# Kernel optimization log

Hardware: AMD Instinct MI355X
Metric: run time of the kernel (lower is better)

The kernel has to match this reference:

```python
import jax, jax.numpy as jnp
import numpy as np

B, C, H, W = 512, 256, 9, 9
HEADS, K = 4, 9
D_K = C // HEADS
EPS = 1e-5


def setup_inputs() -> dict:
    key = jax.random.key(0)
    ks = jax.random.split(key, 8)
    s = 1.0 / np.sqrt(C)
    return {
        "x": jax.random.normal(ks[0], (B, C, H, W), jnp.float32),
        "wq": jax.random.normal(ks[1], (C, C), jnp.float32) * s,
        "bq": jax.random.normal(ks[2], (C,), jnp.float32) * s,
        "wk": jax.random.normal(ks[3], (C, C), jnp.float32) * s,
        "bk": jax.random.normal(ks[4], (C,), jnp.float32) * s,
        "wv": jax.random.normal(ks[5], (C, C), jnp.float32) * s,
        "bv": jax.random.normal(ks[6], (C,), jnp.float32) * s,
        "a": jax.random.normal(ks[7], (HEADS, D_K), jnp.float32),
        "gamma": jnp.ones((C,), jnp.float32),
        "beta": jnp.zeros((C,), jnp.float32),
    }


def reference(x, wq, bq, wk, bk, wv, bv, a, gamma, beta):
    N = H * W  # 81 tokens
    tokens = x.reshape(B, C, N).transpose(0, 2, 1)  # [B, N, C]

    # pairwise euclidean distances (cdist)
    sq = jnp.sum(tokens * tokens, axis=-1)  # [B, N]
    d2 = sq[:, :, None] + sq[:, None, :] - 2.0 * jnp.einsum("bnc,bmc->bnm", tokens, tokens)
    dist = jnp.sqrt(jnp.maximum(d2, 0.0))  # [B, N, N]

    # k nearest neighbors (smallest distance)
    _, idx = jax.lax.top_k(-dist, K)  # idx: [B, N, K]

    # gather neighbor features: [B, N, K, C]
    nbr = jax.vmap(lambda t, i: t[i])(tokens, idx)

    q = tokens @ wq.T + bq                      # [B, N, C]
    kf = nbr @ wk.T + bk                        # [B, N, K, C]
    comb = jax.nn.leaky_relu(q[:, :, None, :] + kf, 0.2)
    comb = comb.reshape(B, N, K, HEADS, D_K)
    scores = jnp.einsum("bnkhd,hd->bnkh", comb, a)
    attn = jax.nn.softmax(scores, axis=2)       # over K neighbors
    v = (nbr @ wv.T + bv).reshape(B, N, K, HEADS, D_K)
    out = jnp.einsum("bnkh,bnkhd->bnhd", attn, v).reshape(B, N, C)
    out = out.transpose(0, 2, 1).reshape(B, C, H, W)

    # BatchNorm2d (training-mode batch statistics, biased variance)
    mean = jnp.mean(out, axis=(0, 2, 3))
    var = jnp.var(out, axis=(0, 2, 3))
    bn = (out - mean[None, :, None, None]) * jax.lax.rsqrt(var + EPS)[None, :, None, None]
    bn = bn * gamma[None, :, None, None] + beta[None, :, None, None]
    return jax.nn.relu(bn + x)
```

## Files before the change

### kernel.cpp

```cpp
#include <hip/hip_runtime.h>
#include <hip/hip_bf16.h>

#define B_   512
#define C_   256
#define N_   81
#define M_   (B_ * N_)
#define KNN  9

typedef __attribute__((ext_vector_type(8))) short short8;
typedef __attribute__((ext_vector_type(4))) float f32x4;
typedef __attribute__((ext_vector_type(4))) ushort u16x4;

#define GLD16(g, l) __builtin_amdgcn_global_load_lds(                      \
    (const __attribute__((address_space(1))) void*)(g),                    \
    (__attribute__((address_space(3))) void*)(l), 16, 0, 0)

__device__ __forceinline__ float bf2f(ushort u) {
  union { uint i; float f; } c; c.i = (uint)u << 16; return c.f;
}
__device__ __forceinline__ ushort f2bf(float f) {
  __hip_bfloat16 h = __float2bfloat16(f); return *(ushort*)&h;
}

__global__ __launch_bounds__(256) void split_kernel(
    const float* __restrict__ x, ushort* __restrict__ tokb,
    char* __restrict__ lobuf,
    const float* __restrict__ wq, const float* __restrict__ bq,
    const float* __restrict__ wk, const float* __restrict__ bk,
    const float* __restrict__ wv, const float* __restrict__ bv,
    ushort* __restrict__ wcat, float* __restrict__ bcat) {
  __shared__ __align__(16) float raw[32 * 81];
  const int bid = blockIdx.x;
  const int tid = threadIdx.x;
  if (bid >= 4096) {
    const int j = bid - 4096, c = tid;
    const int sel = j >> 8, jr = j & 255;
    const float* W  = sel == 0 ? wq : (sel == 1 ? wk : wv);
    const float* Bb = sel == 0 ? bq : (sel == 1 ? bk : bv);
    wcat[(size_t)j * 256 + c] = f2bf(W[jr * 256 + c]);
    if (c == 0) bcat[j] = Bb[jr];
    return;
  }
  const int b = bid >> 3, ch = bid & 7;
  const float* src = x + (size_t)b * (C_ * N_) + ch * 32 * N_;
#pragma unroll
  for (int it = 0; it < 3; ++it) {
    int e4 = tid + it * 256;
    if (e4 < 648) *(f32x4*)&raw[e4 * 4] = *(const f32x4*)&src[e4 * 4];
  }
  char* dst = lobuf + (size_t)bid * 6144;
  __syncthreads();
#pragma unroll
  for (int it = 0; it < 6; ++it) {
    int p = tid + it * 256;
    if (p < 1296) {
      int n = p >> 4, q = p & 15;
      float v0 = raw[(2 * q) * N_ + n];
      float v1 = raw[(2 * q + 1) * N_ + n];
      __hip_bfloat16 h0 = __float2bfloat16(v0);
      __hip_bfloat16 h1 = __float2bfloat16(v1);
      float r0 = v0 - __bfloat162float(h0);
      float r1 = v1 - __bfloat162float(h1);
      __hip_bfloat16 g0 = __float2bfloat16(r0);
      __hip_bfloat16 g1 = __float2bfloat16(r1);
      uint hp = (uint)(*(ushort*)&h0) | ((uint)(*(ushort*)&h1) << 16);
      uint lp = (uint)(*(ushort*)&g0) | ((uint)(*(ushort*)&g1) << 16);
      int off = (((q >> 2) << 4) ^ (((n >> 1) & 3) << 4)) + ((q & 3) << 2);
      *(uint*)(dst + n * 64 + off) = lp;
      *(uint*)&tokb[((size_t)(b * N_ + n)) * 256 + ch * 32 + 2 * q] = hp;
    }
  }
}

__global__ __launch_bounds__(256) void knn_gemm_kernel(
    const ushort* __restrict__ tokb, const char* __restrict__ lobuf,
    int* __restrict__ knn_idx,
    const ushort* __restrict__ wcat, const float* __restrict__ bcat,
    ushort* __restrict__ qkvb) {
  __shared__ __align__(16) char smem[32768];
  const int bid0 = blockIdx.x;
  const int tid = threadIdx.x;
  const int w = tid >> 6, lane = tid & 63;
  const int l15 = lane & 15;

  if (bid0 < B_) {
    float* sqv = (float*)(smem + 31488);
    const int b = bid0;
    const int wr = w >> 1, wc = w & 1;
    const int g16 = lane >> 4;

    const char* tb = (const char*)(tokb + (size_t)b * N_ * 256);
    const char* lb = lobuf + (size_t)b * 8 * 6144;

#pragma unroll
    for (int it = 0; it < 3; ++it) {
      int idx = it * 256 + tid;
      if (idx < 384) {
        int n = idx >> 2, gp = idx & 3;
        int g = gp ^ ((n >> 1) & 3);
        GLD16(tb + (size_t)n * 512 + (g << 4), smem + idx * 16);
      } else {
        GLD16(lb + (idx - 384) * 16, smem + idx * 16);
      }
    }

    f32x4 acc[3][3];
#pragma unroll
    for (int i = 0; i < 3; ++i)
#pragma unroll
      for (int j = 0; j < 3; ++j) acc[i][j] = {0.f, 0.f, 0.f, 0.f};

#pragma unroll
    for (int ch = 0; ch < 8; ++ch) {
      char* cur = smem + (ch & 1) * 12288;
      char* nxt = smem + ((ch + 1) & 1) * 12288;
      if (ch < 7) {
#pragma unroll
        for (int it = 0; it < 3; ++it) {
          int idx = it * 256 + tid;
          if (idx < 384) {
            int n = idx >> 2, gp = idx & 3;
            int g = gp ^ ((n >> 1) & 3);
            GLD16(tb + (size_t)n * 512 + (ch + 1) * 64 + (g << 4),
                  nxt + idx * 16);
          } else {
            GLD16(lb + (size_t)(ch + 1) * 6144 + (idx - 384) * 16,
                  nxt + idx * 16);
          }
        }
        asm volatile("s_waitcnt vmcnt(3)" ::: "memory");
      } else {
        asm volatile("s_waitcnt vmcnt(0)" ::: "memory");
      }
      __builtin_amdgcn_s_barrier();
      __builtin_amdgcn_sched_barrier(0);
      short8 ah[3], al[3], bh[3], bl[3];
#pragma unroll
      for (int i = 0; i < 3; ++i) {
        int ra = wr * 48 + i * 16 + l15;
        int oa = ra * 64 + ((g16 << 4) ^ (((ra >> 1) & 3) << 4));
        ah[i] = *(const short8*)(cur + oa);
        al[i] = *(const short8*)(cur + 6144 + oa);
        int rb = wc * 48 + i * 16 + l15;
        int ob = rb * 64 + ((g16 << 4) ^ (((rb >> 1) & 3) << 4));
        bh[i] = *(const short8*)(cur + ob);
        bl[i] = *(const short8*)(cur + 6144 + ob);
      }
#pragma unroll
      for (int i = 0; i < 3; ++i)
#pragma unroll
        for (int j = 0; j < 3; ++j) {
          acc[i][j] = __builtin_amdgcn_mfma_f32_16x16x32_bf16(
              ah[i], bh[j], acc[i][j], 0, 0, 0);
          acc[i][j] = __builtin_amdgcn_mfma_f32_16x16x32_bf16(
              ah[i], bl[j], acc[i][j], 0, 0, 0);
          acc[i][j] = __builtin_amdgcn_mfma_f32_16x16x32_bf16(
              al[i], bh[j], acc[i][j], 0, 0, 0);
          acc[i][j] = __builtin_amdgcn_mfma_f32_16x16x32_bf16(
              al[i], bl[j], acc[i][j], 0, 0, 0);
        }
      __builtin_amdgcn_sched_barrier(0);
      __builtin_amdgcn_s_barrier();
    }
    float* G = (float*)smem;
#pragma unroll
    for (int i = 0; i < 3; ++i) {
      const int row0 = wr * 48 + i * 16 + ((lane >> 4) << 2);
#pragma unroll
      for (int j = 0; j < 3; ++j) {
        const int col = wc * 48 + j * 16 + l15;
#pragma unroll
        for (int reg = 0; reg < 4; ++reg) {
          const int row = row0 + reg;
          if (row < N_) G[row * 97 + col] = acc[i][j][reg];
        }
      }
    }
    __syncthreads();
    if (tid < N_) sqv[tid] = G[tid * 97 + tid];
    __syncthreads();
    if (tid < N_) {
      const int n = tid;
      const float sn = sqv[n];
      const float* grow = &G[n * 97];
      float bd[KNN]; int bi[KNN];
#pragma unroll
      for (int k = 0; k < KNN; ++k) { bd[k] = 3.4e38f; bi[k] = 0; }
      for (int m = 0; m < N_; ++m) {
        float d2 = sn + sqv[m] - 2.f * grow[m];
        float wv = bd[0]; int wi = 0;
#pragma unroll
        for (int k = 1; k < KNN; ++k) {
          bool g_ = bd[k] > wv;
          wv = g_ ? bd[k] : wv;
          wi = g_ ? k : wi;
        }
        bool repl = d2 < wv;
#pragma unroll
        for (int k = 0; k < KNN; ++k) {
          bool here = repl & (wi == k);
          bd[k] = here ? d2 : bd[k];
          bi[k] = here ? m : bi[k];
        }
      }
#pragma unroll
      for (int k = 0; k < KNN; ++k)
        knn_idx[((size_t)b * N_ + n) * KNN + k] = bi[k];
    }
    return;
  }

  ushort* At = (ushort*)smem;
  ushort* Bt = (ushort*)(smem + 16384);
  const int bid = bid0 - B_;
  const int xcd = bid & 7, li = bid >> 3;
  const int mt = xcd * 41 + li / 6;
  if (mt >= 324) return;
  const int m0 = mt * 128;
  const int j0 = (li % 6) * 128;
  const int wr = w >> 1, wc = w & 1;

  const char* pA[4]; const char* pB[4]; int oL[4];
#pragma unroll
  for (int it = 0; it < 4; ++it) {
    int o = (it * 256 + tid) * 16;
    int r = o >> 7, cp = o & 127;
    int cl = cp ^ ((r & 7) << 4);
    oL[it] = o;
    pA[it] = (const char*)tokb + ((size_t)(m0 + r) * 256) * 2 + cl;
    pB[it] = (const char*)wcat + ((size_t)(j0 + r) * 256) * 2 + cl;
  }

  f32x4 acc[4][4];
#pragma unroll
  for (int i = 0; i < 4; ++i)
#pragma unroll
    for (int j = 0; j < 4; ++j) acc[i][j] = {0.f, 0.f, 0.f, 0.f};

  const int sw = (lane & 7) << 4;
  const int kgrp = (lane >> 4) << 4;

  for (int k0 = 0; k0 < 256; k0 += 64) {
    __syncthreads();
#pragma unroll
    for (int it = 0; it < 4; ++it) {
      GLD16(pA[it] + k0 * 2, (char*)At + oL[it]);
      GLD16(pB[it] + k0 * 2, (char*)Bt + oL[it]);
    }
    __syncthreads();
#pragma unroll
    for (int kk = 0; kk < 2; ++kk) {
      const int cb = (kk * 64 + kgrp) ^ sw;
      short8 am[4], bn[4];
#pragma unroll
      for (int i = 0; i < 4; ++i) {
        const int ra = wr * 64 + i * 16 + l15;
        am[i] = *(const short8*)((const char*)At + ra * 128 + cb);
        const int rb = wc * 64 + i * 16 + l15;
        bn[i] = *(const short8*)((const char*)Bt + rb * 128 + cb);
      }
#pragma unroll
      for (int i = 0; i < 4; ++i)
#pragma unroll
        for (int j = 0; j < 4; ++j)
          acc[i][j] = __builtin_amdgcn_mfma_f32_16x16x32_bf16(
              am[i], bn[j], acc[i][j], 0, 0, 0);
    }
  }

#pragma unroll
  for (int j = 0; j < 4; ++j) {
    const int colj = j0 + wc * 64 + j * 16 + l15;
    const float bs = bcat[colj];
#pragma unroll
    for (int i = 0; i < 4; ++i) {
      const int rowm = m0 + wr * 64 + i * 16 + ((lane >> 4) << 2);
#pragma unroll
      for (int reg = 0; reg < 4; ++reg)
        qkvb[(size_t)(rowm + reg) * 768 + colj] = f2bf(acc[i][j][reg] + bs);
    }
  }
}

__global__ __launch_bounds__(256) void attn_kernel(
    const ushort* __restrict__ qkvc, const int* __restrict__ knn_idx,
    const float* __restrict__ a, ushort* __restrict__ qkvb) {
  const int nwg = M_ / 4;
  const int bid = blockIdx.x;
  const int swz = (bid & 7) * (nwg / 8) + (bid >> 3);
  const int w = threadIdx.x >> 6, lane = threadIdx.x & 63;
  const int m = swz * 4 + w;
  const int b = m / N_;
  const int bbase = b * N_;

  int nbk_l = 0;
  if (lane < KNN) nbk_l = knn_idx[(size_t)m * KNN + lane];

  const u16x4 qu = *(const u16x4*)&qkvc[(size_t)m * 768 + lane * 4];
  const f32x4 a4 = *(const f32x4*)&a[lane * 4];
  float q4[4];
#pragma unroll
  for (int u = 0; u < 4; ++u) q4[u] = bf2f(qu[u]);

  u16x4 ku[KNN], vu[KNN];
#pragma unroll
  for (int k = 0; k < KNN; ++k) {
    const int nbk = __builtin_amdgcn_readlane(nbk_l, k);
    const ushort* row = qkvc + (size_t)(bbase + nbk) * 768;
    ku[k] = *(const u16x4*)&row[256 + lane * 4];
    vu[k] = *(const u16x4*)&row[512 + lane * 4];
  }

  float sc[KNN];
#pragma unroll
  for (int k = 0; k < KNN; ++k) {
    float p = 0.f;
#pragma unroll
    for (int u = 0; u < 4; ++u) {
      float t = q4[u] + bf2f(ku[k][u]);
      t = fmaxf(t, 0.2f * t);
      p = __builtin_fmaf(t, a4[u], p);
    }
    p += __shfl_xor(p, 1, 16);
    p += __shfl_xor(p, 2, 16);
    p += __shfl_xor(p, 4, 16);
    p += __shfl_xor(p, 8, 16);
    sc[k] = p;
  }
  float mx = sc[0];
#pragma unroll
  for (int k = 1; k < KNN; ++k) mx = fmaxf(mx, sc[k]);
  float s = 0.f;
#pragma unroll
  for (int k = 0; k < KNN; ++k) {
    sc[k] = __builtin_amdgcn_exp2f((sc[k] - mx) * 1.44269504f);
    s += sc[k];
  }
  const float inv = __builtin_amdgcn_rcpf(s);
  f32x4 acc = {0.f, 0.f, 0.f, 0.f};
#pragma unroll
  for (int k = 0; k < KNN; ++k) {
    const float wk_ = sc[k] * inv;
#pragma unroll
    for (int u = 0; u < 4; ++u)
      acc[u] = __builtin_fmaf(wk_, bf2f(vu[k][u]), acc[u]);
  }
  u16x4 o;
#pragma unroll
  for (int u = 0; u < 4; ++u) o[u] = f2bf(acc[u]);
  *(u16x4*)&qkvb[(size_t)m * 768 + lane * 4] = o;
}

__global__ __launch_bounds__(256) void bn_partial_kernel(
    const ushort* __restrict__ qkvb, float* __restrict__ ps,
    float* __restrict__ ps2) {
  const int g = blockIdx.x, c = threadIdx.x;
  float s = 0.f, s2 = 0.f;
  for (int r = 0; r < M_ / 256; ++r) {
    float v = bf2f(qkvb[((size_t)g * (M_ / 256) + r) * 768 + c]);
    s += v; s2 += v * v;
  }
  ps[g * 256 + c] = s;
  ps2[g * 256 + c] = s2;
}

__global__ __launch_bounds__(256) void bn_finalize_kernel(
    const float* __restrict__ ps, const float* __restrict__ ps2,
    const float* __restrict__ gamma, const float* __restrict__ beta,
    float* __restrict__ scale, float* __restrict__ shift) {
  __shared__ float red[2][256];
  const int c = blockIdx.x, t = threadIdx.x;
  red[0][t] = ps[t * 256 + c];
  red[1][t] = ps2[t * 256 + c];
  __syncthreads();
#pragma unroll
  for (int off = 128; off > 0; off >>= 1) {
    if (t < off) {
      red[0][t] += red[0][t + off];
      red[1][t] += red[1][t + off];
    }
    __syncthreads();
  }
  if (t == 0) {
    const float mean = red[0][0] * (1.f / (float)M_);
    const float var = red[1][0] * (1.f / (float)M_) - mean * mean;
    const float rstd = rsqrtf(var + 1e-5f);
    scale[c] = gamma[c] * rstd;
    shift[c] = beta[c] - mean * gamma[c] * rstd;
  }
}

__global__ __launch_bounds__(256) void bn_apply_kernel(
    const ushort* __restrict__ qkvb, const float* __restrict__ x,
    const float* __restrict__ scale, const float* __restrict__ shift,
    float* __restrict__ y) {
  __shared__ float t[N_ * 65];
  const int b = blockIdx.x, tid = threadIdx.x;
  for (int c0 = 0; c0 < 256; c0 += 64) {
    __syncthreads();
    for (int e = tid; e < N_ * 64; e += 256) {
      int n = e >> 6, c = e & 63;
      t[n * 65 + c] = bf2f(qkvb[((size_t)b * N_ + n) * 768 + c0 + c]);
    }
    __syncthreads();
    for (int f = tid; f < 64 * N_; f += 256) {
      int c = f / N_, n = f - c * N_;
      float o = t[n * 65 + c];
      size_t gi = (size_t)b * (C_ * N_) + (size_t)(c0 + c) * N_ + n;
      float bn = o * scale[c0 + c] + shift[c0 + c];
      float v = bn + x[gi];
      y[gi] = v > 0.f ? v : 0.f;
    }
  }
}

extern "C" void kernel_launch(void* const* d_in, const int* in_sizes, int n_in,
                              void* d_out, int out_size, void* d_ws,
                              size_t ws_size, hipStream_t stream) {
  const float* x     = (const float*)d_in[0];
  const float* wq    = (const float*)d_in[1];
  const float* bq    = (const float*)d_in[2];
  const float* wk    = (const float*)d_in[3];
  const float* bk    = (const float*)d_in[4];
  const float* wv    = (const float*)d_in[5];
  const float* bv    = (const float*)d_in[6];
  const float* a     = (const float*)d_in[7];
  const float* gamma = (const float*)d_in[8];
  const float* beta  = (const float*)d_in[9];
  float* out = (float*)d_out;

  ushort* qkvb = (ushort*)d_ws;
  char*   lobuf = (char*)qkvb;
  ushort* tokb = qkvb + (size_t)M_ * 768;
  ushort* wcat = tokb + (size_t)M_ * 256;
  float*  bcat = (float*)(wcat + 768 * 256);
  int*    kidx = (int*)(bcat + 768);
  float*  ps   = (float*)(kidx + (size_t)M_ * KNN);
  float*  ps2  = ps + 256 * 256;
  float*  scale = ps2 + 256 * 256;
  float*  shift = scale + 256;
  char*   lobuf2 = (char*)(shift + 256);

  split_kernel<<<4096 + 768, 256, 0, stream>>>(
      x, tokb, lobuf2, wq, bq, wk, bk, wv, bv, wcat, bcat);
  knn_gemm_kernel<<<B_ + 1968, 256, 0, stream>>>(
      tokb, lobuf2, kidx, wcat, bcat, qkvb);
  attn_kernel<<<M_ / 4, 256, 0, stream>>>(qkvb, kidx, a, qkvb);
  bn_partial_kernel<<<256, 256, 0, stream>>>(qkvb, ps, ps2);
  bn_finalize_kernel<<<256, 256, 0, stream>>>(ps, ps2, gamma, beta, scale, shift);
  bn_apply_kernel<<<B_, 256, 0, stream>>>(qkvb, x, scale, shift, out);
}
```

Baseline: 141.1 us.

## Double-buffer QKV GEMM LDS tiles with 32-wide K chunks and async prefetch

The QKV projection GEMM used a single LDS buffer with 64-wide K steps and two full barriers per step. It now splits K into eight 32-wide chunks in two ping-pong LDS buffers. The next chunk is issued with global_load_lds before waiting on the current one through explicit vmcnt and s_barrier. This aims to overlap global loads with MFMA work, at the cost of more barrier rounds and a new XOR swizzle that must stay correct.

```diff
diff --git a/kernel.cpp b/kernel.cpp
--- a/kernel.cpp
+++ b/kernel.cpp
@@ -210,8 +210,6 @@
     return;
   }
 
-  ushort* At = (ushort*)smem;
-  ushort* Bt = (ushort*)(smem + 16384);
   const int bid = bid0 - B_;
   const int xcd = bid & 7, li = bid >> 3;
   const int mt = xcd * 41 + li / 6;
@@ -220,15 +218,15 @@
   const int j0 = (li % 6) * 128;
   const int wr = w >> 1, wc = w & 1;
 
-  const char* pA[4]; const char* pB[4]; int oL[4];
-#pragma unroll
-  for (int it = 0; it < 4; ++it) {
-    int o = (it * 256 + tid) * 16;
-    int r = o >> 7, cp = o & 127;
-    int cl = cp ^ ((r & 7) << 4);
-    oL[it] = o;
-    pA[it] = (const char*)tokb + ((size_t)(m0 + r) * 256) * 2 + cl;
-    pB[it] = (const char*)wcat + ((size_t)(j0 + r) * 256) * 2 + cl;
+  const char* pA[2]; const char* pB[2]; int oL[2];
+#pragma unroll
+  for (int it = 0; it < 2; ++it) {
+    int s = tid + it * 256;
+    int r = s >> 2, gp = s & 3;
+    int gl = (gp ^ (r & 3)) << 4;
+    oL[it] = s * 16;
+    pA[it] = (const char*)tokb + (size_t)(m0 + r) * 512 + gl;
+    pB[it] = (const char*)wcat + (size_t)(j0 + r) * 512 + gl;
   }
 
   f32x4 acc[4][4];
@@ -237,35 +235,49 @@
 #pragma unroll
     for (int j = 0; j < 4; ++j) acc[i][j] = {0.f, 0.f, 0.f, 0.f};
 
-  const int sw = (lane & 7) << 4;
   const int kgrp = (lane >> 4) << 4;
 
-  for (int k0 = 0; k0 < 256; k0 += 64) {
-    __syncthreads();
-#pragma unroll
-    for (int it = 0; it < 4; ++it) {
-      GLD16(pA[it] + k0 * 2, (char*)At + oL[it]);
-      GLD16(pB[it] + k0 * 2, (char*)Bt + oL[it]);
-    }
-    __syncthreads();
-#pragma unroll
-    for (int kk = 0; kk < 2; ++kk) {
-      const int cb = (kk * 64 + kgrp) ^ sw;
-      short8 am[4], bn[4];
-#pragma unroll
-      for (int i = 0; i < 4; ++i) {
-        const int ra = wr * 64 + i * 16 + l15;
-        am[i] = *(const short8*)((const char*)At + ra * 128 + cb);
-        const int rb = wc * 64 + i * 16 + l15;
-        bn[i] = *(const short8*)((const char*)Bt + rb * 128 + cb);
-      }
-#pragma unroll
-      for (int i = 0; i < 4; ++i)
-#pragma unroll
-        for (int j = 0; j < 4; ++j)
-          acc[i][j] = __builtin_amdgcn_mfma_f32_16x16x32_bf16(
-              am[i], bn[j], acc[i][j], 0, 0, 0);
-    }
+#pragma unroll
+  for (int it = 0; it < 2; ++it) {
+    GLD16(pA[it], smem + oL[it]);
+    GLD16(pB[it], smem + 16384 + oL[it]);
+  }
+
+  for (int ch = 0; ch < 8; ++ch) {
+    const int cur = ch & 1;
+    char* Ac = smem + cur * 8192;
+    char* Bc = smem + 16384 + cur * 8192;
+    if (ch < 7) {
+      char* An = smem + (cur ^ 1) * 8192;
+      char* Bn = smem + 16384 + (cur ^ 1) * 8192;
+      const int ko = (ch + 1) * 64;
+#pragma unroll
+      for (int it = 0; it < 2; ++it) {
+        GLD16(pA[it] + ko, An + oL[it]);
+        GLD16(pB[it] + ko, Bn + oL[it]);
+      }
+      asm volatile("s_waitcnt vmcnt(4)" ::: "memory");
+    } else {
+      asm volatile("s_waitcnt vmcnt(0)" ::: "memory");
+    }
+    __builtin_amdgcn_s_barrier();
+    __builtin_amdgcn_sched_barrier(0);
+    short8 am[4], bn[4];
+#pragma unroll
+    for (int i = 0; i < 4; ++i) {
+      const int ra = wr * 64 + i * 16 + l15;
+      am[i] = *(const short8*)(Ac + ra * 64 + (kgrp ^ ((ra & 3) << 4)));
+      const int rb = wc * 64 + i * 16 + l15;
+      bn[i] = *(const short8*)(Bc + rb * 64 + (kgrp ^ ((rb & 3) << 4)));
+    }
+#pragma unroll
+    for (int i = 0; i < 4; ++i)
+#pragma unroll
+      for (int j = 0; j < 4; ++j)
+        acc[i][j] = __builtin_amdgcn_mfma_f32_16x16x32_bf16(
+            am[i], bn[j], acc[i][j], 0, 0, 0);
+    __builtin_amdgcn_sched_barrier(0);
+    __builtin_amdgcn_s_barrier();
   }
 
 #pragma unroll
@@ -430,7 +442,6 @@
   float* out = (float*)d_out;
 
   ushort* qkvb = (ushort*)d_ws;
-  char*   lobuf = (char*)qkvb;
   ushort* tokb = qkvb + (size_t)M_ * 768;
   ushort* wcat = tokb + (size_t)M_ * 256;
   float*  bcat = (float*)(wcat + 768 * 256);
```

Measured after the change: 143.3 us. About the same (+1.6%).
